# Optimization experiments

Hardware: AMD Instinct MI355X
Metric: run time of the kernel (lower is better)

The kernel has to match this reference:

```python
import jax, jax.numpy as jnp
import numpy as np
import math

MAX_L = 3
E, R, C = 100000, 8, 16  # num_edges, n_radial, n_chanel


def _l_list(max_l):
    # all monomial exponent triples (lx,ly,lz) with lx+ly+lz <= max_l,
    # in the nested-loop order used for init_kwargs l_list
    return [(lx, ly, lz)
            for lx in range(max_l + 1)
            for ly in range(max_l + 1 - lx)
            for lz in range(max_l + 1 - lx - ly)]


def _combo_indices(max_l):
    # find_combo_vectors_l1l2: for every l3 in l_list, every componentwise
    # decomposition l3 = l1 + l2, with integer binomial prefactor
    ll = _l_list(max_l)
    idx = {t: i for i, t in enumerate(ll)}
    l3s, l1s, l2s, pf = [], [], [], []
    for l3 in ll:
        for a in range(l3[0] + 1):
            for b in range(l3[1] + 1):
                for c in range(l3[2] + 1):
                    l1 = (a, b, c)
                    l2 = (l3[0] - a, l3[1] - b, l3[2] - c)
                    l3s.append(idx[l3])
                    l1s.append(idx[l1])
                    l2s.append(idx[l2])
                    pf.append(math.comb(l3[0], a) * math.comb(l3[1], b) * math.comb(l3[2], c))
    return (np.asarray(l3s, np.int32), np.asarray(l1s, np.int32),
            np.asarray(l2s, np.int32), np.asarray(pf, np.float32))


def setup_inputs() -> dict:
    key = jax.random.key(0)
    k1, k2 = jax.random.split(key)
    A = len(_l_list(MAX_L))  # n_angular = 20
    edge_attr1 = jax.random.normal(k1, (E, R, A, C), dtype=jnp.float32)
    edge_attr2 = jax.random.normal(k2, (E, R, A, C), dtype=jnp.float32)
    l3_idx, l1_idx, l2_idx, prefactor = _combo_indices(MAX_L)
    return {
        "edge_attr1": edge_attr1,
        "edge_attr2": edge_attr2,
        "l3_idx": jnp.asarray(l3_idx),
        "l1_idx": jnp.asarray(l1_idx),
        "l2_idx": jnp.asarray(l2_idx),
        "prefactor": jnp.asarray(prefactor),
    }


def reference(edge_attr1, edge_attr2, l3_idx, l1_idx, l2_idx, prefactor):
    # vectorized gather-multiply-scale over all K=84 (l1,l2,l3) combos,
    # then one scatter-add into the l3 angular slot
    terms = (prefactor[None, None, :, None]
             * edge_attr1[:, :, l1_idx, :]
             * edge_attr2[:, :, l2_idx, :])  # [E, R, K, C]
    out = jnp.zeros_like(edge_attr1).at[:, :, l3_idx, :].add(terms)
    return out
```

## Files before the change

### kernel.cpp

```cpp
#include <hip/hip_runtime.h>


#define NA 20
#define NK 84

namespace atp {

constexpr int lidx(int x, int y, int z) {
  int i = 0;
  for (int a = 0; a < x; ++a) i += (4 - a) * (5 - a) / 2;
  for (int b = 0; b < y; ++b) i += 4 - x - b;
  return i + z;
}

constexpr int combi(int n, int k) {
  int r = 1;
  for (int i = 1; i <= k; ++i) r = r * (n - k + i) / i;
  return r;
}

struct Tab {
  int l1[NK];
  int l2[NK];
  float pf[NK];
  int cnt[NA];
  int off[NA];
};

constexpr Tab make_tab() {
  Tab t{};
  int n = 0, m = 0;
  for (int x = 0; x <= 3; ++x)
    for (int y = 0; y <= 3 - x; ++y)
      for (int z = 0; z <= 3 - x - y; ++z) {
        t.off[m] = n;
        t.cnt[m] = (x + 1) * (y + 1) * (z + 1);
        for (int a = 0; a <= x; ++a)
          for (int b = 0; b <= y; ++b)
            for (int c = 0; c <= z; ++c) {
              t.l1[n] = lidx(a, b, c);
              t.l2[n] = lidx(x - a, y - b, z - c);
              t.pf[n] = (float)(combi(x, a) * combi(y, b) * combi(z, c));
              ++n;
            }
        ++m;
      }
  return t;
}

constexpr Tab T = make_tab();

}

__global__ __launch_bounds__(256) void atp_kernel(
    const float* __restrict__ in1, const float* __restrict__ in2,
    float* __restrict__ out, int n_pairs) {
  const int tid = blockIdx.x * 256 + threadIdx.x;
  if (tid >= n_pairs) return;
  const int er = tid >> 3;
  const int c2 = tid & 7;

  const float2* p1 = reinterpret_cast<const float2*>(in1) + er * (NA * 8) + c2;
  const float2* p2 = reinterpret_cast<const float2*>(in2) + er * (NA * 8) + c2;
  float2* po = reinterpret_cast<float2*>(out) + er * (NA * 8) + c2;

  float2 v1[NA], v2[NA];
#pragma unroll
  for (int a = 0; a < NA; ++a) v1[a] = p1[a * 8];
#pragma unroll
  for (int a = 0; a < NA; ++a) v2[a] = p2[a * 8];

#pragma unroll
  for (int i3 = 0; i3 < NA; ++i3) {
    float2 acc = make_float2(0.f, 0.f);
#pragma unroll
    for (int j = 0; j < atp::T.cnt[i3]; ++j) {
      const int k = atp::T.off[i3] + j;
      const float pf = atp::T.pf[k];
      const float2 a = v1[atp::T.l1[k]];
      const float2 b = v2[atp::T.l2[k]];
      acc.x = fmaf(pf * a.x, b.x, acc.x);
      acc.y = fmaf(pf * a.y, b.y, acc.y);
    }
    po[i3 * 8] = acc;
  }
}

extern "C" void kernel_launch(void* const* d_in, const int* in_sizes, int n_in,
                              void* d_out, int out_size, void* d_ws, size_t ws_size,
                              hipStream_t stream) {
  const float* in1 = (const float*)d_in[0];
  const float* in2 = (const float*)d_in[1];
  float* out = (float*)d_out;
  const int n_pairs = out_size / NA / 2;
  const int blocks = (n_pairs + 255) / 256;
  atp_kernel<<<blocks, 256, 0, stream>>>(in1, in2, out, n_pairs);
}
```

Before: 609.3 us.

## Stage tiles through LDS for fully coalesced 16-byte global loads and stores

Each 128-thread block now copies 8 (edge,radial) rows of both inputs into padded shared memory using contiguous float4 global loads. Each thread then computes one channel from LDS and writes its results back to LDS, and the block stores them with coalesced float4 writes. The goal is to replace the strided float2 accesses, where each thread hit 20 separate 64-byte-spaced addresses, with streaming vector memory transactions. The cost is extra LDS traffic and barriers, and the bounds check was removed, so the grid assumes the size divides evenly into tiles.

```diff
diff --git a/kernel.cpp b/kernel.cpp
--- a/kernel.cpp
+++ b/kernel.cpp
@@ -3,6 +3,12 @@
 
 #define NA 20
 #define NK 84
+#define TR 8
+#define ROWQ 80
+#define PADQ 82
+#define NTH 128
+
+typedef float f32x4 __attribute__((ext_vector_type(4)));
 
 namespace atp {
 
@@ -52,37 +58,62 @@
 
 }
 
-__global__ __launch_bounds__(256) void atp_kernel(
+__global__ __launch_bounds__(NTH) void atp_kernel(
     const float* __restrict__ in1, const float* __restrict__ in2,
-    float* __restrict__ out, int n_pairs) {
-  const int tid = blockIdx.x * 256 + threadIdx.x;
-  if (tid >= n_pairs) return;
-  const int er = tid >> 3;
-  const int c2 = tid & 7;
+    float* __restrict__ out) {
+  __shared__ f32x4 lds1[TR * PADQ];
+  __shared__ f32x4 lds2[TR * PADQ];
 
-  const float2* p1 = reinterpret_cast<const float2*>(in1) + er * (NA * 8) + c2;
-  const float2* p2 = reinterpret_cast<const float2*>(in2) + er * (NA * 8) + c2;
-  float2* po = reinterpret_cast<float2*>(out) + er * (NA * 8) + c2;
+  const int t = threadIdx.x;
+  const long base_q = (long)blockIdx.x * (TR * ROWQ);
+  const f32x4* g1 = reinterpret_cast<const f32x4*>(in1) + base_q;
+  const f32x4* g2 = reinterpret_cast<const f32x4*>(in2) + base_q;
+  f32x4* go = reinterpret_cast<f32x4*>(out) + base_q;
 
-  float2 v1[NA], v2[NA];
 #pragma unroll
-  for (int a = 0; a < NA; ++a) v1[a] = p1[a * 8];
+  for (int k = 0; k < 5; ++k) {
+    const int q = k * NTH + t;
+    const int row = q / ROWQ;
+    const int qq = q - row * ROWQ;
+    lds1[row * PADQ + qq] = g1[q];
+    lds2[row * PADQ + qq] = g2[q];
+  }
+  __syncthreads();
+
+  const int row = t >> 4;
+  const int c = t & 15;
+  const float* l1p = reinterpret_cast<const float*>(lds1) + row * (PADQ * 4) + c;
+  const float* l2p = reinterpret_cast<const float*>(lds2) + row * (PADQ * 4) + c;
+
+  float v1[NA], v2[NA], o[NA];
 #pragma unroll
-  for (int a = 0; a < NA; ++a) v2[a] = p2[a * 8];
+  for (int a = 0; a < NA; ++a) v1[a] = l1p[a * 16];
+#pragma unroll
+  for (int a = 0; a < NA; ++a) v2[a] = l2p[a * 16];
 
 #pragma unroll
   for (int i3 = 0; i3 < NA; ++i3) {
-    float2 acc = make_float2(0.f, 0.f);
+    float acc = 0.f;
 #pragma unroll
     for (int j = 0; j < atp::T.cnt[i3]; ++j) {
       const int k = atp::T.off[i3] + j;
-      const float pf = atp::T.pf[k];
-      const float2 a = v1[atp::T.l1[k]];
-      const float2 b = v2[atp::T.l2[k]];
-      acc.x = fmaf(pf * a.x, b.x, acc.x);
-      acc.y = fmaf(pf * a.y, b.y, acc.y);
+      acc = fmaf(atp::T.pf[k] * v1[atp::T.l1[k]], v2[atp::T.l2[k]], acc);
     }
-    po[i3 * 8] = acc;
+    o[i3] = acc;
+  }
+  __syncthreads();
+
+  float* lop = reinterpret_cast<float*>(lds1) + row * (PADQ * 4) + c;
+#pragma unroll
+  for (int a = 0; a < NA; ++a) lop[a * 16] = o[a];
+  __syncthreads();
+
+#pragma unroll
+  for (int k = 0; k < 5; ++k) {
+    const int q = k * NTH + t;
+    const int row2 = q / ROWQ;
+    const int qq = q - row2 * ROWQ;
+    go[q] = lds1[row2 * PADQ + qq];
   }
 }
 
@@ -92,7 +123,6 @@
   const float* in1 = (const float*)d_in[0];
   const float* in2 = (const float*)d_in[1];
   float* out = (float*)d_out;
-  const int n_pairs = out_size / NA / 2;
-  const int blocks = (n_pairs + 255) / 256;
-  atp_kernel<<<blocks, 256, 0, stream>>>(in1, in2, out, n_pairs);
+  const int n_tiles = out_size / (TR * NA * 16);
+  atp_kernel<<<n_tiles, NTH, 0, stream>>>(in1, in2, out);
 }
```

After: 578.4 us. 1.05x faster.
